# Optimization experiments

Hardware: AMD Instinct MI355X
Metric: run time of the kernel (lower is better)

Reference implementation:

```python
import jax, jax.numpy as jnp
import numpy as np

B, T, IN, OUT, H, N, M = 16, 1024, 64, 64, 512, 128, 40
EPS = 1e-8


def setup_inputs() -> dict:
    key = jax.random.key(0)
    ks = jax.random.split(key, 16)
    s = 0.02  # xavier-ish init scale for weights
    inp = {
        "x": jax.random.normal(ks[0], (B, T, IN), jnp.float32),
        "h0": jnp.zeros((B, H), jnp.float32),
        "c0": jnp.zeros((B, H), jnp.float32),
        "memory0": jax.random.normal(ks[1], (B, N, M), jnp.float32) * 0.01,
        "read0": jnp.zeros((B, M), jnp.float32),
        # LSTMCell params (torch gate order: i, f, g, o)
        "W_ih": jax.random.normal(ks[2], (4 * H, IN + M), jnp.float32) * s,
        "b_ih": jnp.zeros((4 * H,), jnp.float32),
        "W_hh": jax.random.normal(ks[3], (4 * H, H), jnp.float32) * s,
        "b_hh": jnp.zeros((4 * H,), jnp.float32),
        "W_fc": jax.random.normal(ks[4], (OUT, H), jnp.float32) * s,
        "b_fc": jnp.zeros((OUT,), jnp.float32),
        "W_e": jax.random.normal(ks[5], (M, H), jnp.float32) * s,
        "b_e": jnp.zeros((M,), jnp.float32),
        "W_a": jax.random.normal(ks[6], (M, H), jnp.float32) * s,
        "b_a": jnp.zeros((M,), jnp.float32),
        "W_k": jax.random.normal(ks[7], (M, H), jnp.float32) * s,
        "b_k": jnp.zeros((M,), jnp.float32),
        "W_b": jax.random.normal(ks[8], (1, H), jnp.float32) * s,
        "b_b": jnp.zeros((1,), jnp.float32),
    }
    return inp


def _ntm_scan(x, h0, c0, memory0, read0, W_ih, b_ih, W_hh, b_hh,
              W_fc, b_fc, W_e, b_e, W_a, b_a, W_k, b_k, W_b, b_b):
    def step(carry, x_t):
        h, c, mem, r = carry
        # controller LSTM cell on [x_t, read_vector]
        inp = jnp.concatenate([x_t, r], axis=-1)            # [B, IN+M]
        gates = inp @ W_ih.T + b_ih + h @ W_hh.T + b_hh      # [B, 4H]
        i, f, g, o = jnp.split(gates, 4, axis=-1)
        i = jax.nn.sigmoid(i); f = jax.nn.sigmoid(f)
        g = jnp.tanh(g);       o = jax.nn.sigmoid(o)
        c = f * c + i * g
        h = o * jnp.tanh(c)
        out = jnp.tanh(h @ W_fc.T + b_fc)                    # [B, OUT]
        # content addressing
        key = jnp.tanh(h @ W_k.T + b_k)                      # [B, M]
        beta = jax.nn.softplus(h @ W_b.T + b_b) + EPS        # [B, 1]
        kn = key / (jnp.linalg.norm(key, axis=-1, keepdims=True) + EPS)
        mn = mem / (jnp.linalg.norm(mem, axis=-1, keepdims=True) + EPS)
        sim = jnp.einsum('bnm,bm->bn', mn, kn)               # [B, N]
        w = jax.nn.softmax(beta * sim, axis=-1)              # [B, N]
        # erase/add write, then read from updated memory
        e = jax.nn.sigmoid(h @ W_e.T + b_e)                  # [B, M]
        a = jnp.tanh(h @ W_a.T + b_a)                        # [B, M]
        mem = mem * (1.0 - w[:, :, None] * e[:, None, :]) + w[:, :, None] * a[:, None, :]
        r = jnp.einsum('bn,bnm->bm', w, mem)                 # [B, M]
        return (h, c, mem, r), out

    xs = jnp.swapaxes(x, 0, 1)                               # [T, B, IN]
    (h, c, mem, r), outs = jax.lax.scan(step, (h0, c0, memory0, read0), xs)
    return jnp.swapaxes(outs, 0, 1), h, c                    # [B, T, OUT]


def reference(x, h0, c0, memory0, read0, W_ih, b_ih, W_hh, b_hh,
              W_fc, b_fc, W_e, b_e, W_a, b_a, W_k, b_k, W_b, b_b):
    return _ntm_scan(x, h0, c0, memory0, read0, W_ih, b_ih, W_hh, b_hh,
                     W_fc, b_fc, W_e, b_e, W_a, b_a, W_k, b_k, W_b, b_b)
```

## Files before the change

kernel.cpp:

```cpp
#include <hip/hip_runtime.h>
#include <math.h>

#define Bq   16
#define Tq   1024
#define OUTq 64
#define Hq   512
#define Nq   128
#define Mq   40
#define NT   512
#define NISL 16
#define GWG  13
#define IWG  14
#define NWG  224
#define EPSq 1e-8f
#define MAGIC 0x00C0FFEEu

typedef unsigned long long ull;

__device__ __forceinline__ float sigmf(float x){ return 1.f/(1.f + expf(-x)); }
__device__ __forceinline__ float softplusf(float x){ return (x > 20.f) ? x : log1pf(expf(x)); }

__device__ __forceinline__ ull icld64(const ull* p){
  return __hip_atomic_load(p, __ATOMIC_RELAXED, __HIP_MEMORY_SCOPE_AGENT);
}
__device__ __forceinline__ void icst64(ull* p, ull v){
  __hip_atomic_store(p, v, __ATOMIC_RELAXED, __HIP_MEMORY_SCOPE_AGENT);
}
__device__ __forceinline__ ull icpoll64(const ull* p){
  ull v;
  asm volatile("global_load_dwordx2 %0, %1, off sc0 sc1\n\ts_waitcnt vmcnt(0)"
               : "=v"(v) : "v"(p) : "memory");
  return v;
}
__device__ __forceinline__ ull packtv(unsigned tag, float v){
  return ((ull)tag << 32) | (ull)__float_as_uint(v);
}
__device__ __forceinline__ float lowf(ull v){ return __uint_as_float((unsigned)v); }

__device__ __forceinline__ float waitword(const ull* sh, unsigned want, bool fast){
  if (fast){
    #pragma unroll 1
    for (int i = 0; i < 4096; ++i){
      const ull v = icpoll64(sh);
      if ((unsigned)(v >> 32) == want) return lowf(v);
      __builtin_amdgcn_s_sleep(1);
    }
  }
  #pragma unroll 1
  for (;;){
    const ull v = icld64(sh);
    if ((unsigned)(v >> 32) == want) return lowf(v);
    __builtin_amdgcn_s_sleep(1);
  }
}

__device__ __forceinline__ int ready_and_handshake(ull* rdy, ull* magic, int blk){
  __hip_atomic_fetch_add(rdy, 1ull, __ATOMIC_RELAXED, __HIP_MEMORY_SCOPE_AGENT);
  while (icld64(rdy) < (ull)NWG) __builtin_amdgcn_s_sleep(8);
  if (blk == 0) icst64(magic, ((ull)MAGIC << 32) | 1ull);
  #pragma unroll 1
  for (int i = 0; i < 4000; ++i){
    if ((unsigned)(icpoll64(magic) >> 32) == MAGIC) return 1;
    __builtin_amdgcn_s_sleep(2);
  }
  return 0;
}

extern "C" __global__ void __launch_bounds__(NT, 1)
ntm_kernel(const float* __restrict__ xg,  const float* __restrict__ h0g,
           const float* __restrict__ c0g, const float* __restrict__ mem0g,
           const float* __restrict__ read0g,
           const float* __restrict__ Wih, const float* __restrict__ bih,
           const float* __restrict__ Whh, const float* __restrict__ bhh,
           const float* __restrict__ Wfc, const float* __restrict__ bfc,
           const float* __restrict__ We,  const float* __restrict__ be,
           const float* __restrict__ Wa,  const float* __restrict__ ba,
           const float* __restrict__ Wk,  const float* __restrict__ bk,
           const float* __restrict__ Wb,  const float* __restrict__ bbeta,
           float* __restrict__ yout, ull* __restrict__ rdy,
           ull* __restrict__ h_sh, ull* __restrict__ r_sh)
{
  const int blk = blockIdx.x;
  const int tid = threadIdx.x;
  const int x   = blk & 7;
  const int j   = blk >> 3;
  const int bat = (j < IWG) ? x : (x + 8);
  const int slot= (j < IWG) ? j : (j - IWG);
  __shared__ __align__(16) char smem[41344];
  __shared__ int s_fast;
  ull* magic = rdy + 1;

  if (slot < GWG){
    float* inp_s  = (float*)smem;
    float* red_s  = (float*)(smem + 2560);
    float* rw_s   = (float*)(smem + 13440);
    float* r_s    = (float*)(smem + 39680);
    float* gate_s = (float*)(smem + 39840);
    float* c_s    = (float*)(smem + 40480);
    float* bias_s = (float*)(smem + 40640);

    const int kseg  = tid & 15;
    const int rslot = tid >> 4;
    const int nd    = (slot < 12) ? 40 : 32;
    const int d0    = slot * 40;
    const int rowsR = 4 * nd;

    float4 w4[5][9];
    #pragma unroll
    for (int rr = 0; rr < 5; ++rr){
      const int row = rslot*5 + rr;
      if (row < rowsR){
        const int gate = row / nd, ld = row - gate*nd;
        const int grow = gate*Hq + d0 + ld;
        #pragma unroll
        for (int kk = 0; kk < 9; ++kk){
          float v[4];
          #pragma unroll
          for (int c4 = 0; c4 < 4; ++c4){
            const int k = kseg*36 + kk*4 + c4;
            v[c4] = (k < 64) ? Wih[grow*104 + k] : Whh[grow*512 + (k - 64)];
          }
          w4[rr][kk] = make_float4(v[0], v[1], v[2], v[3]);
        }
      } else {
        #pragma unroll
        for (int kk = 0; kk < 9; ++kk) w4[rr][kk] = make_float4(0.f,0.f,0.f,0.f);
      }
    }
    if (tid < rowsR){
      const int gate = tid / nd, ld = tid - gate*nd;
      const int grow = gate*Hq + d0 + ld;
      bias_s[tid] = bih[grow] + bhh[grow];
    }
    for (int i = tid; i < rowsR*40; i += NT){
      const int row = i / 40, m = i - row*40;
      const int gate = row / nd, ld = row - gate*nd;
      const int grow = gate*Hq + d0 + ld;
      rw_s[row*41 + m] = Wih[grow*104 + 64 + m];
    }
    if (tid < nd) c_s[tid] = c0g[bat*Hq + d0 + tid];
    if (tid < 16)
      *(float4*)&inp_s[tid*4] = ((const float4*)xg)[(bat*Tq + 0)*16 + tid];
    if (tid < 128)
      *(float4*)&inp_s[64 + tid*4] = ((const float4*)h0g)[bat*128 + tid];
    __syncthreads();
    if (tid == 0) s_fast = ready_and_handshake(rdy, magic, blk);
    __syncthreads();
    const bool fast = (s_fast != 0);

    for (int t = 0; t < Tq; ++t){
      const int p = t & 1, pm = (t - 1) & 1;
      float acc[5] = {0.f,0.f,0.f,0.f,0.f};
      {
        const float* bp = inp_s + kseg*36;
        #pragma unroll
        for (int kk = 0; kk < 9; ++kk){
          const float4 f = *(const float4*)&bp[kk*4];
          #pragma unroll
          for (int rr = 0; rr < 5; ++rr)
            acc[rr] += w4[rr][kk].x*f.x + w4[rr][kk].y*f.y
                     + w4[rr][kk].z*f.z + w4[rr][kk].w*f.w;
        }
      }
      #pragma unroll
      for (int rr = 0; rr < 5; ++rr)
        red_s[(rslot*5 + rr)*17 + kseg] = acc[rr];
      if (t == 0){
        if (tid < 40) r_s[tid] = read0g[bat*Mq + tid];
      } else if (tid < 40){
        const int idx = (pm*NISL + bat)*Mq + tid;
        r_s[tid] = waitword(&r_sh[idx], (unsigned)t, fast);
      }
      __syncthreads();
      if (tid < rowsR){
        float s2 = bias_s[tid];
        const float* rp = &red_s[tid*17];
        #pragma unroll
        for (int q = 0; q < 16; ++q) s2 += rp[q];
        const float* rwp = &rw_s[tid*41];
        #pragma unroll
        for (int m = 0; m < 40; ++m) s2 += rwp[m]*r_s[m];
        gate_s[tid] = s2;
      }
      __syncthreads();
      if (tid < nd){
        const float gi = gate_s[tid];
        const float gf = gate_s[nd + tid];
        const float gc = gate_s[2*nd + tid];
        const float go = gate_s[3*nd + tid];
        const float iv = sigmf(gi), fv = sigmf(gf), gv = tanhf(gc), ov = sigmf(go);
        const float cn = fv*c_s[tid] + iv*gv;
        const float hn = ov*tanhf(cn);
        c_s[tid] = cn;
        const int idx = (p*NISL + bat)*Hq + d0 + tid;
        icst64(&h_sh[idx], packtv((unsigned)(t+1), hn));
        if (t == Tq - 1){
          yout[Bq*Tq*OUTq + bat*Hq + d0 + tid] = hn;
          yout[Bq*Tq*OUTq + Bq*Hq + bat*Hq + d0 + tid] = cn;
        }
      }
      {
        const int idx = (p*NISL + bat)*Hq + tid;
        inp_s[64 + tid] = waitword(&h_sh[idx], (unsigned)(t+1), fast);
      }
      if (t + 1 < Tq && tid < 16)
        *(float4*)&inp_s[tid*4] = ((const float4*)xg)[(bat*Tq + t + 1)*16 + tid];
      __syncthreads();
    }
  }
  else {
    float* mem_s  = (float*)smem;
    float* h_s    = (float*)(smem + 22528);
    float* hred_s = (float*)(smem + 24576);
    float* key_s  = (float*)(smem + 26624);
    float* e_s    = (float*)(smem + 26784);
    float* a_s    = (float*)(smem + 26944);
    float* w_s    = (float*)(smem + 27104);
    float* rred_s = (float*)(smem + 27616);
    float* ored_s = (float*)(smem + 29056);

    #pragma unroll
    for (int q = 0; q < 10; ++q){
      const int e = q*512 + tid;
      const int n = e / 40, m = e - n*40;
      mem_s[n*44 + m] = mem0g[bat*(Nq*Mq) + e];
    }
    const int o  = tid & 127;
    const int kc = tid >> 7;
    const float* wrow = (o < 40) ? (Wk + o*Hq)
                      : (o < 80) ? (We + (o-40)*Hq)
                      : (o < 120) ? (Wa + (o-80)*Hq)
                      : (o == 120) ? Wb : nullptr;
    float4 wv2[32];
    if (wrow){
      #pragma unroll
      for (int kk = 0; kk < 32; ++kk)
        wv2[kk] = *(const float4*)&wrow[kc*128 + kk*4];
    } else {
      #pragma unroll
      for (int kk = 0; kk < 32; ++kk) wv2[kk] = make_float4(0.f,0.f,0.f,0.f);
    }
    float4 wfc[16];
    {
      const int o2 = tid & 63, kc8 = tid >> 6;
      #pragma unroll
      for (int kk = 0; kk < 16; ++kk)
        wfc[kk] = *(const float4*)&Wfc[o2*Hq + kc8*64 + kk*4];
    }
    const float bfcv = bfc[tid & 63];
    float hb0 = 0.f, hb1 = 0.f;
    if (tid < 64){
      const int o0 = tid, o1 = tid + 64;
      hb0 = (o0 < 40) ? bk[o0] : be[o0-40];
      hb1 = (o1 < 80) ? be[o1-40] : (o1 < 120) ? ba[o1-80]
          : (o1 == 120) ? bbeta[0] : 0.f;
    }
    __syncthreads();
    if (tid == 0) s_fast = ready_and_handshake(rdy, magic, blk);
    __syncthreads();
    const bool fast = (s_fast != 0);

    for (int t = 0; t < Tq; ++t){
      const int p = t & 1;
      const unsigned want = (unsigned)(t + 1);
      {
        const int idx = (p*NISL + bat)*Hq + tid;
        h_s[tid] = waitword(&h_sh[idx], want, fast);
      }
      __syncthreads();
      {
        float a0 = 0.f;
        const float* hp = h_s + kc*128;
        #pragma unroll
        for (int kk = 0; kk < 32; ++kk){
          const float4 f = *(const float4*)&hp[kk*4];
          a0 += wv2[kk].x*f.x + wv2[kk].y*f.y + wv2[kk].z*f.z + wv2[kk].w*f.w;
        }
        hred_s[o*4 + kc] = a0;
      }
      __syncthreads();
      if (tid < 64){
        const int l = tid;
        const float4 p0 = *(const float4*)&hred_s[l*4];
        const float4 p1 = *(const float4*)&hred_s[(l+64)*4];
        float s0 = hb0 + p0.x + p0.y + p0.z + p0.w;
        float s1 = hb1 + p1.x + p1.y + p1.z + p1.w;
        float kv = 0.f;
        if (l < 40){ kv = tanhf(s0); key_s[l] = kv; }
        else        { e_s[l-40] = sigmf(s0); }
        if (l < 16)      e_s[l+24]  = sigmf(s1);
        else if (l < 56) a_s[l-16]  = tanhf(s1);
        float bval = softplusf(s1) + EPSq;
        const float bet = __shfl(bval, 56);
        float ss = kv*kv;
        #pragma unroll
        for (int off = 32; off; off >>= 1) ss += __shfl_xor(ss, off);
        const float rinv = 1.f/(sqrtf(ss) + EPSq);
        float sc[2];
        #pragma unroll
        for (int half = 0; half < 2; ++half){
          const int n = l + 64*half;
          float qq = 0.f, dd = 0.f;
          const float* mrow = &mem_s[n*44];
          #pragma unroll
          for (int q = 0; q < 10; ++q){
            const float4 mv = *(const float4*)&mrow[q*4];
            const float4 kvv = *(const float4*)&key_s[q*4];
            qq += mv.x*mv.x + mv.y*mv.y + mv.z*mv.z + mv.w*mv.w;
            dd += mv.x*kvv.x + mv.y*kvv.y + mv.z*kvv.z + mv.w*kvv.w;
          }
          sc[half] = bet * dd * rinv / (sqrtf(qq) + EPSq);
        }
        const float e0 = expf(sc[0]), e1 = expf(sc[1]);
        float sm = e0 + e1;
        #pragma unroll
        for (int off = 32; off; off >>= 1) sm += __shfl_xor(sm, off);
        const float inv = 1.f/sm;
        w_s[l] = e0*inv; w_s[l+64] = e1*inv;
      }
      __syncthreads();
      if (tid < 320){
        const int m = tid % 40, ng = tid / 40;
        const float ev = e_s[m], av = a_s[m];
        float part = 0.f;
        #pragma unroll
        for (int q = 0; q < 16; ++q){
          const int n = ng*16 + q, idx2 = n*44 + m;
          const float mv = mem_s[idx2];
          const float wn = w_s[n];
          const float nv = fmaf(wn, fmaf(-ev, mv, av), mv);
          mem_s[idx2] = nv;
          part = fmaf(wn, nv, part);
        }
        rred_s[m*9 + ng] = part;
      }
      __syncthreads();
      if (tid < 40){
        float r = 0.f;
        #pragma unroll
        for (int q = 0; q < 8; ++q) r += rred_s[tid*9 + q];
        const int idx = (p*NISL + bat)*Mq + tid;
        icst64(&r_sh[idx], packtv(want, r));
      }
      {
        const int o2 = tid & 63, kc8 = tid >> 6;
        float a0 = 0.f;
        const float* hp = h_s + kc8*64;
        #pragma unroll
        for (int kk = 0; kk < 16; ++kk){
          const float4 f = *(const float4*)&hp[kk*4];
          a0 += wfc[kk].x*f.x + wfc[kk].y*f.y + wfc[kk].z*f.z + wfc[kk].w*f.w;
        }
        ored_s[o2*9 + kc8] = a0;
      }
      __syncthreads();
      if (tid < 64){
        float s2 = bfcv;
        const float* op = &ored_s[tid*9];
        #pragma unroll
        for (int q = 0; q < 8; ++q) s2 += op[q];
        yout[(bat*Tq + t)*OUTq + tid] = tanhf(s2);
      }
      __syncthreads();
    }
  }
}

extern "C" void kernel_launch(void* const* d_in, const int* in_sizes, int n_in,
                              void* d_out, int out_size, void* d_ws, size_t ws_size,
                              hipStream_t stream){
  const float* xg    = (const float*)d_in[0];
  const float* h0g   = (const float*)d_in[1];
  const float* c0g   = (const float*)d_in[2];
  const float* mem0g = (const float*)d_in[3];
  const float* read0g= (const float*)d_in[4];
  const float* Wih   = (const float*)d_in[5];
  const float* bih   = (const float*)d_in[6];
  const float* Whh   = (const float*)d_in[7];
  const float* bhh   = (const float*)d_in[8];
  const float* Wfc   = (const float*)d_in[9];
  const float* bfc   = (const float*)d_in[10];
  const float* We    = (const float*)d_in[11];
  const float* be    = (const float*)d_in[12];
  const float* Wa    = (const float*)d_in[13];
  const float* ba    = (const float*)d_in[14];
  const float* Wk    = (const float*)d_in[15];
  const float* bk    = (const float*)d_in[16];
  const float* Wb    = (const float*)d_in[17];
  const float* bbeta = (const float*)d_in[18];

  float* yout  = (float*)d_out;
  ull*   rdy   = (ull*)d_ws;
  ull*   h_sh  = (ull*)((char*)d_ws + 4096);
  ull*   r_sh  = (ull*)((char*)d_ws + 135168);

  hipMemsetAsync(d_ws, 0, 147456, stream);
  hipLaunchKernelGGL(ntm_kernel, dim3(NWG), dim3(NT), 0, stream,
                     xg, h0g, c0g, mem0g, read0g, Wih, bih, Whh, bhh,
                     Wfc, bfc, We, be, Wa, ba, Wk, bk, Wb, bbeta,
                     yout, rdy, h_sh, r_sh);
}
```

Before: 6.419 ms.

## Compute head projections as partial sums in LSTM workgroups, reduce in memory workgroup

Each gate workgroup now computes partial dot products of its own slice of h with the key/erase/add/beta weight rows and publishes them to a new global flag-tagged buffer. The memory workgroup sums the 13 partials instead of waiting for the full h and doing the 512-wide projection, which shortens the critical recurrent path. The full-h wait moves later, used only for the output FC, and one trailing barrier is dropped. This adds an extra block barrier and more global atomic stores in the gate workgroups, plus 13 polls per projection row.

```diff
diff --git a/kernel.cpp b/kernel.cpp
--- a/kernel.cpp
+++ b/kernel.cpp
@@ -78,7 +78,8 @@
            const float* __restrict__ Wk,  const float* __restrict__ bk,
            const float* __restrict__ Wb,  const float* __restrict__ bbeta,
            float* __restrict__ yout, ull* __restrict__ rdy,
-           ull* __restrict__ h_sh, ull* __restrict__ r_sh)
+           ull* __restrict__ h_sh, ull* __restrict__ r_sh,
+           ull* __restrict__ hp_sh)
 {
   const int blk = blockIdx.x;
   const int tid = threadIdx.x;
@@ -104,6 +105,9 @@
     const int nd    = (slot < 12) ? 40 : 32;
     const int d0    = slot * 40;
     const int rowsR = 4 * nd;
+    const int prow  = tid >> 2;
+    const int pq    = tid & 3;
+    const int ncol  = nd >> 2;
 
     float4 w4[5][9];
     #pragma unroll
@@ -126,6 +130,17 @@
         #pragma unroll
         for (int kk = 0; kk < 9; ++kk) w4[rr][kk] = make_float4(0.f,0.f,0.f,0.f);
       }
+    }
+    float hw[10];
+    #pragma unroll
+    for (int c = 0; c < 10; ++c) hw[c] = 0.f;
+    if (prow < 121){
+      const float* wsrc = (prow < 40) ? (Wk + prow*Hq)
+                        : (prow < 80) ? (We + (prow-40)*Hq)
+                        : (prow < 120) ? (Wa + (prow-80)*Hq) : Wb;
+      #pragma unroll
+      for (int c = 0; c < 10; ++c)
+        if (c < ncol) hw[c] = wsrc[d0 + pq*ncol + c];
     }
     if (tid < rowsR){
       const int gate = tid / nd, ld = tid - gate*nd;
@@ -192,11 +207,25 @@
         const float cn = fv*c_s[tid] + iv*gv;
         const float hn = ov*tanhf(cn);
         c_s[tid] = cn;
+        r_s[tid] = hn;
         const int idx = (p*NISL + bat)*Hq + d0 + tid;
         icst64(&h_sh[idx], packtv((unsigned)(t+1), hn));
         if (t == Tq - 1){
           yout[Bq*Tq*OUTq + bat*Hq + d0 + tid] = hn;
           yout[Bq*Tq*OUTq + Bq*Hq + bat*Hq + d0 + tid] = cn;
+        }
+      }
+      __syncthreads();
+      {
+        float ps = 0.f;
+        #pragma unroll
+        for (int c = 0; c < 10; ++c)
+          if (c < ncol) ps = fmaf(hw[c], r_s[pq*ncol + c], ps);
+        ps += __shfl_xor(ps, 1);
+        ps += __shfl_xor(ps, 2);
+        if (prow < 121 && pq == 0){
+          const int hidx = ((p*NISL + bat)*GWG + slot)*128 + prow;
+          icst64(&hp_sh[hidx], packtv((unsigned)(t+1), ps));
         }
       }
       {
@@ -225,21 +254,8 @@
       const int n = e / 40, m = e - n*40;
       mem_s[n*44 + m] = mem0g[bat*(Nq*Mq) + e];
     }
-    const int o  = tid & 127;
-    const int kc = tid >> 7;
-    const float* wrow = (o < 40) ? (Wk + o*Hq)
-                      : (o < 80) ? (We + (o-40)*Hq)
-                      : (o < 120) ? (Wa + (o-80)*Hq)
-                      : (o == 120) ? Wb : nullptr;
-    float4 wv2[32];
-    if (wrow){
-      #pragma unroll
-      for (int kk = 0; kk < 32; ++kk)
-        wv2[kk] = *(const float4*)&wrow[kc*128 + kk*4];
-    } else {
-      #pragma unroll
-      for (int kk = 0; kk < 32; ++kk) wv2[kk] = make_float4(0.f,0.f,0.f,0.f);
-    }
+    const int prow_m = tid & 127;
+    const int psg    = tid >> 7;
     float4 wfc[16];
     {
       const int o2 = tid & 63, kc8 = tid >> 6;
@@ -263,20 +279,18 @@
     for (int t = 0; t < Tq; ++t){
       const int p = t & 1;
       const unsigned want = (unsigned)(t + 1);
-      {
-        const int idx = (p*NISL + bat)*Hq + tid;
-        h_s[tid] = waitword(&h_sh[idx], want, fast);
-      }
-      __syncthreads();
-      {
-        float a0 = 0.f;
-        const float* hp = h_s + kc*128;
-        #pragma unroll
-        for (int kk = 0; kk < 32; ++kk){
-          const float4 f = *(const float4*)&hp[kk*4];
-          a0 += wv2[kk].x*f.x + wv2[kk].y*f.y + wv2[kk].z*f.z + wv2[kk].w*f.w;
-        }
-        hred_s[o*4 + kc] = a0;
+      if (prow_m < 121){
+        const int sbase = (psg == 0) ? 0 : (psg*3 + 1);
+        const int scnt  = (psg == 0) ? 4 : 3;
+        float s = 0.f;
+        #pragma unroll
+        for (int ss = 0; ss < 4; ++ss){
+          if (ss < scnt){
+            const int hidx = ((p*NISL + bat)*GWG + (sbase + ss))*128 + prow_m;
+            s += waitword(&hp_sh[hidx], want, fast);
+          }
+        }
+        hred_s[prow_m*4 + psg] = s;
       }
       __syncthreads();
       if (tid < 64){
@@ -343,6 +357,11 @@
         icst64(&r_sh[idx], packtv(want, r));
       }
       {
+        const int idx = (p*NISL + bat)*Hq + tid;
+        h_s[tid] = waitword(&h_sh[idx], want, fast);
+      }
+      __syncthreads();
+      {
         const int o2 = tid & 63, kc8 = tid >> 6;
         float a0 = 0.f;
         const float* hp = h_s + kc8*64;
@@ -361,7 +380,6 @@
         for (int q = 0; q < 8; ++q) s2 += op[q];
         yout[(bat*Tq + t)*OUTq + tid] = tanhf(s2);
       }
-      __syncthreads();
     }
   }
 }
@@ -393,10 +411,11 @@
   ull*   rdy   = (ull*)d_ws;
   ull*   h_sh  = (ull*)((char*)d_ws + 4096);
   ull*   r_sh  = (ull*)((char*)d_ws + 135168);
-
-  hipMemsetAsync(d_ws, 0, 147456, stream);
+  ull*   hp_sh = (ull*)((char*)d_ws + 147456);
+
+  hipMemsetAsync(d_ws, 0, 573440, stream);
   hipLaunchKernelGGL(ntm_kernel, dim3(NWG), dim3(NT), 0, stream,
                      xg, h0g, c0g, mem0g, read0g, Wih, bih, Whh, bhh,
                      Wfc, bfc, We, be, Wa, ba, Wk, bk, Wb, bbeta,
-                     yout, rdy, h_sh, r_sh);
-}
+                     yout, rdy, h_sh, r_sh, hp_sh);
+}
```

New measurement: 6.982 ms. 8.8% more time.

## Replace per-word tagged handoff with packed data plus per-batch arrival counters

Applied to the files above, without the earlier changes.

Cross-workgroup exchange of h and the read vector used to put a step tag next to every float, so each consumer polled every word. Now two floats share each 64-bit word and producers bump a per-batch atomic counter after a vmcnt wait. Consumers poll one counter, then read the packed data once. This cuts the traffic and polling on the serial critical path. It depends on ordering between the data stores and the counter increment, and it also drops a trailing __syncthreads in the memory workgroup.

```diff
diff --git a/kernel.cpp b/kernel.cpp
--- a/kernel.cpp
+++ b/kernel.cpp
@@ -32,26 +32,31 @@
                : "=v"(v) : "v"(p) : "memory");
   return v;
 }
-__device__ __forceinline__ ull packtv(unsigned tag, float v){
-  return ((ull)tag << 32) | (ull)__float_as_uint(v);
+__device__ __forceinline__ ull rd64(const ull* p, bool fast){
+  return fast ? icpoll64(p) : icld64(p);
+}
+__device__ __forceinline__ ull pack2(float lo, float hi){
+  return ((ull)__float_as_uint(hi) << 32) | (ull)__float_as_uint(lo);
 }
 __device__ __forceinline__ float lowf(ull v){ return __uint_as_float((unsigned)v); }
-
-__device__ __forceinline__ float waitword(const ull* sh, unsigned want, bool fast){
+__device__ __forceinline__ float highf(ull v){ return __uint_as_float((unsigned)(v >> 32)); }
+
+__device__ __forceinline__ void pollcnt(const ull* c, ull target, bool fast){
   if (fast){
     #pragma unroll 1
-    for (int i = 0; i < 4096; ++i){
-      const ull v = icpoll64(sh);
-      if ((unsigned)(v >> 32) == want) return lowf(v);
+    for (int i = 0; i < (1 << 22); ++i){
+      if (icpoll64(c) >= target) return;
       __builtin_amdgcn_s_sleep(1);
     }
   }
   #pragma unroll 1
   for (;;){
-    const ull v = icld64(sh);
-    if ((unsigned)(v >> 32) == want) return lowf(v);
+    if (icld64(c) >= target) return;
     __builtin_amdgcn_s_sleep(1);
   }
+}
+__device__ __forceinline__ void cntbump(ull* c){
+  __hip_atomic_fetch_add(c, 1ull, __ATOMIC_RELAXED, __HIP_MEMORY_SCOPE_AGENT);
 }
 
 __device__ __forceinline__ int ready_and_handshake(ull* rdy, ull* magic, int blk){
@@ -78,7 +83,8 @@
            const float* __restrict__ Wk,  const float* __restrict__ bk,
            const float* __restrict__ Wb,  const float* __restrict__ bbeta,
            float* __restrict__ yout, ull* __restrict__ rdy,
-           ull* __restrict__ h_sh, ull* __restrict__ r_sh)
+           ull* __restrict__ h_dat, ull* __restrict__ r_dat,
+           ull* __restrict__ h_cnt, ull* __restrict__ r_cnt)
 {
   const int blk = blockIdx.x;
   const int tid = threadIdx.x;
@@ -89,6 +95,8 @@
   __shared__ __align__(16) char smem[41344];
   __shared__ int s_fast;
   ull* magic = rdy + 1;
+  ull* hc = h_cnt + bat*16;
+  ull* rc = r_cnt + bat*16;
 
   if (slot < GWG){
     float* inp_s  = (float*)smem;
@@ -167,9 +175,12 @@
         red_s[(rslot*5 + rr)*17 + kseg] = acc[rr];
       if (t == 0){
         if (tid < 40) r_s[tid] = read0g[bat*Mq + tid];
-      } else if (tid < 40){
-        const int idx = (pm*NISL + bat)*Mq + tid;
-        r_s[tid] = waitword(&r_sh[idx], (unsigned)t, fast);
+      } else {
+        pollcnt(rc, (ull)t, fast);
+        if (tid < 20){
+          const ull w = rd64(&r_dat[(pm*NISL + bat)*32 + tid], fast);
+          r_s[2*tid] = lowf(w); r_s[2*tid + 1] = highf(w);
+        }
       }
       __syncthreads();
       if (tid < rowsR){
@@ -183,25 +194,33 @@
         gate_s[tid] = s2;
       }
       __syncthreads();
-      if (tid < nd){
-        const float gi = gate_s[tid];
-        const float gf = gate_s[nd + tid];
-        const float gc = gate_s[2*nd + tid];
-        const float go = gate_s[3*nd + tid];
-        const float iv = sigmf(gi), fv = sigmf(gf), gv = tanhf(gc), ov = sigmf(go);
-        const float cn = fv*c_s[tid] + iv*gv;
-        const float hn = ov*tanhf(cn);
-        c_s[tid] = cn;
-        const int idx = (p*NISL + bat)*Hq + d0 + tid;
-        icst64(&h_sh[idx], packtv((unsigned)(t+1), hn));
-        if (t == Tq - 1){
-          yout[Bq*Tq*OUTq + bat*Hq + d0 + tid] = hn;
-          yout[Bq*Tq*OUTq + Bq*Hq + bat*Hq + d0 + tid] = cn;
-        }
-      }
-      {
-        const int idx = (p*NISL + bat)*Hq + tid;
-        inp_s[64 + tid] = waitword(&h_sh[idx], (unsigned)(t+1), fast);
+      if (tid < 64){
+        float hn = 0.f;
+        if (tid < nd){
+          const float gi = gate_s[tid];
+          const float gf = gate_s[nd + tid];
+          const float gc = gate_s[2*nd + tid];
+          const float go = gate_s[3*nd + tid];
+          const float iv = sigmf(gi), fv = sigmf(gf), gv = tanhf(gc), ov = sigmf(go);
+          const float cn = fv*c_s[tid] + iv*gv;
+          hn = ov*tanhf(cn);
+          c_s[tid] = cn;
+          if (t == Tq - 1){
+            yout[Bq*Tq*OUTq + bat*Hq + d0 + tid] = hn;
+            yout[Bq*Tq*OUTq + Bq*Hq + bat*Hq + d0 + tid] = cn;
+          }
+        }
+        const float lo = __shfl(hn, 2*tid);
+        const float hi = __shfl(hn, 2*tid + 1);
+        if (tid < (nd >> 1))
+          icst64(&h_dat[(p*NISL + bat)*256 + (d0 >> 1) + tid], pack2(lo, hi));
+        asm volatile("s_waitcnt vmcnt(0)" ::: "memory");
+        if (tid == 0) cntbump(hc);
+      }
+      pollcnt(hc, (ull)(13*(t + 1)), fast);
+      if (tid < 256){
+        const ull w = rd64(&h_dat[(p*NISL + bat)*256 + tid], fast);
+        inp_s[64 + 2*tid] = lowf(w); inp_s[64 + 2*tid + 1] = highf(w);
       }
       if (t + 1 < Tq && tid < 16)
         *(float4*)&inp_s[tid*4] = ((const float4*)xg)[(bat*Tq + t + 1)*16 + tid];
@@ -262,10 +281,10 @@
 
     for (int t = 0; t < Tq; ++t){
       const int p = t & 1;
-      const unsigned want = (unsigned)(t + 1);
-      {
-        const int idx = (p*NISL + bat)*Hq + tid;
-        h_s[tid] = waitword(&h_sh[idx], want, fast);
+      pollcnt(hc, (ull)(13*(t + 1)), fast);
+      if (tid < 256){
+        const ull w = rd64(&h_dat[(p*NISL + bat)*256 + tid], fast);
+        h_s[2*tid] = lowf(w); h_s[2*tid + 1] = highf(w);
       }
       __syncthreads();
       {
@@ -335,12 +354,18 @@
         rred_s[m*9 + ng] = part;
       }
       __syncthreads();
-      if (tid < 40){
+      if (tid < 64){
         float r = 0.f;
-        #pragma unroll
-        for (int q = 0; q < 8; ++q) r += rred_s[tid*9 + q];
-        const int idx = (p*NISL + bat)*Mq + tid;
-        icst64(&r_sh[idx], packtv(want, r));
+        if (tid < 40){
+          #pragma unroll
+          for (int q = 0; q < 8; ++q) r += rred_s[tid*9 + q];
+        }
+        const float lo = __shfl(r, 2*tid);
+        const float hi = __shfl(r, 2*tid + 1);
+        if (tid < 20)
+          icst64(&r_dat[(p*NISL + bat)*32 + tid], pack2(lo, hi));
+        asm volatile("s_waitcnt vmcnt(0)" ::: "memory");
+        if (tid == 0) cntbump(rc);
       }
       {
         const int o2 = tid & 63, kc8 = tid >> 6;
@@ -361,7 +386,6 @@
         for (int q = 0; q < 8; ++q) s2 += op[q];
         yout[(bat*Tq + t)*OUTq + tid] = tanhf(s2);
       }
-      __syncthreads();
     }
   }
 }
@@ -391,12 +415,14 @@
 
   float* yout  = (float*)d_out;
   ull*   rdy   = (ull*)d_ws;
-  ull*   h_sh  = (ull*)((char*)d_ws + 4096);
-  ull*   r_sh  = (ull*)((char*)d_ws + 135168);
-
-  hipMemsetAsync(d_ws, 0, 147456, stream);
+  ull*   h_dat = (ull*)((char*)d_ws + 4096);
+  ull*   r_dat = (ull*)((char*)d_ws + 69632);
+  ull*   h_cnt = (ull*)((char*)d_ws + 77824);
+  ull*   r_cnt = (ull*)((char*)d_ws + 79872);
+
+  hipMemsetAsync(d_ws, 0, 81920, stream);
   hipLaunchKernelGGL(ntm_kernel, dim3(NWG), dim3(NT), 0, stream,
                      xg, h0g, c0g, mem0g, read0g, Wih, bih, Whh, bhh,
                      Wfc, bfc, We, be, Wa, ba, Wk, bk, Wb, bbeta,
-                     yout, rdy, h_sh, r_sh);
-}
+                     yout, rdy, h_dat, r_dat, h_cnt, r_cnt);
+}
```

Measured after the change: 10.23 ms. 1.59x slower.

## Process two batch rows per workgroup, halving the persistent grid

Applied to the files above, without the earlier changes.

Each workgroup now handles two batch elements (pr and pr+8) instead of one, so the grid shrinks from 224 to 112 workgroups. The register-resident weight slices are reused for both batches, shared memory grows to hold duplicated per-batch buffers, and the polling and reduction phases are split across thread halves. This reduces the number of workgroups taking part in the cross-workgroup spin synchronisation each step and doubles weight reuse. The cost is more serial work per workgroup on the critical path of every timestep.

```diff
diff --git a/kernel.cpp b/kernel.cpp
--- a/kernel.cpp
+++ b/kernel.cpp
@@ -11,7 +11,7 @@
 #define NISL 16
 #define GWG  13
 #define IWG  14
-#define NWG  224
+#define NWG  112
 #define EPSq 1e-8f
 #define MAGIC 0x00C0FFEEu
 
@@ -82,22 +82,27 @@
 {
   const int blk = blockIdx.x;
   const int tid = threadIdx.x;
-  const int x   = blk & 7;
+  const int pr  = blk & 7;
   const int j   = blk >> 3;
-  const int bat = (j < IWG) ? x : (x + 8);
-  const int slot= (j < IWG) ? j : (j - IWG);
-  __shared__ __align__(16) char smem[41344];
+  const int batA = pr, batB = pr + 8;
+  const int slot = j;
+  __shared__ __align__(16) char smem[62720];
   __shared__ int s_fast;
   ull* magic = rdy + 1;
 
   if (slot < GWG){
-    float* inp_s  = (float*)smem;
-    float* red_s  = (float*)(smem + 2560);
-    float* rw_s   = (float*)(smem + 13440);
-    float* r_s    = (float*)(smem + 39680);
-    float* gate_s = (float*)(smem + 39840);
-    float* c_s    = (float*)(smem + 40480);
-    float* bias_s = (float*)(smem + 40640);
+    float* inp_sA = (float*)smem;
+    float* inp_sB = (float*)(smem + 2560);
+    float* red_sA = (float*)(smem + 5120);
+    float* red_sB = (float*)(smem + 16000);
+    float* rw_s   = (float*)(smem + 26880);
+    float* r_sA   = (float*)(smem + 53120);
+    float* r_sB   = (float*)(smem + 53280);
+    float* gate_sA= (float*)(smem + 53440);
+    float* gate_sB= (float*)(smem + 54080);
+    float* c_sA   = (float*)(smem + 54720);
+    float* c_sB   = (float*)(smem + 54880);
+    float* bias_s = (float*)(smem + 55040);
 
     const int kseg  = tid & 15;
     const int rslot = tid >> 4;
@@ -138,11 +143,18 @@
       const int grow = gate*Hq + d0 + ld;
       rw_s[row*41 + m] = Wih[grow*104 + 64 + m];
     }
-    if (tid < nd) c_s[tid] = c0g[bat*Hq + d0 + tid];
+    if (tid < nd){
+      c_sA[tid] = c0g[batA*Hq + d0 + tid];
+      c_sB[tid] = c0g[batB*Hq + d0 + tid];
+    }
     if (tid < 16)
-      *(float4*)&inp_s[tid*4] = ((const float4*)xg)[(bat*Tq + 0)*16 + tid];
+      *(float4*)&inp_sA[tid*4] = ((const float4*)xg)[(batA*Tq + 0)*16 + tid];
+    else if (tid < 32)
+      *(float4*)&inp_sB[(tid-16)*4] = ((const float4*)xg)[(batB*Tq + 0)*16 + tid-16];
     if (tid < 128)
-      *(float4*)&inp_s[64 + tid*4] = ((const float4*)h0g)[bat*128 + tid];
+      *(float4*)&inp_sA[64 + tid*4] = ((const float4*)h0g)[batA*128 + tid];
+    else if (tid < 256)
+      *(float4*)&inp_sB[64 + (tid-128)*4] = ((const float4*)h0g)[batB*128 + (tid-128)];
     __syncthreads();
     if (tid == 0) s_fast = ready_and_handshake(rdy, magic, blk);
     __syncthreads();
@@ -150,9 +162,9 @@
 
     for (int t = 0; t < Tq; ++t){
       const int p = t & 1, pm = (t - 1) & 1;
-      float acc[5] = {0.f,0.f,0.f,0.f,0.f};
       {
-        const float* bp = inp_s + kseg*36;
+        float acc[5] = {0.f,0.f,0.f,0.f,0.f};
+        const float* bp = inp_sA + kseg*36;
         #pragma unroll
         for (int kk = 0; kk < 9; ++kk){
           const float4 f = *(const float4*)&bp[kk*4];
@@ -161,69 +173,130 @@
             acc[rr] += w4[rr][kk].x*f.x + w4[rr][kk].y*f.y
                      + w4[rr][kk].z*f.z + w4[rr][kk].w*f.w;
         }
-      }
-      #pragma unroll
-      for (int rr = 0; rr < 5; ++rr)
-        red_s[(rslot*5 + rr)*17 + kseg] = acc[rr];
+        #pragma unroll
+        for (int rr = 0; rr < 5; ++rr)
+          red_sA[(rslot*5 + rr)*17 + kseg] = acc[rr];
+      }
+      {
+        float acc[5] = {0.f,0.f,0.f,0.f,0.f};
+        const float* bp = inp_sB + kseg*36;
+        #pragma unroll
+        for (int kk = 0; kk < 9; ++kk){
+          const float4 f = *(const float4*)&bp[kk*4];
+          #pragma unroll
+          for (int rr = 0; rr < 5; ++rr)
+            acc[rr] += w4[rr][kk].x*f.x + w4[rr][kk].y*f.y
+                     + w4[rr][kk].z*f.z + w4[rr][kk].w*f.w;
+        }
+        #pragma unroll
+        for (int rr = 0; rr < 5; ++rr)
+          red_sB[(rslot*5 + rr)*17 + kseg] = acc[rr];
+      }
       if (t == 0){
-        if (tid < 40) r_s[tid] = read0g[bat*Mq + tid];
-      } else if (tid < 40){
-        const int idx = (pm*NISL + bat)*Mq + tid;
-        r_s[tid] = waitword(&r_sh[idx], (unsigned)t, fast);
+        if (tid < 40) r_sA[tid] = read0g[batA*Mq + tid];
+        else if (tid >= 64 && tid < 104) r_sB[tid-64] = read0g[batB*Mq + (tid-64)];
+      } else {
+        if (tid < 40)
+          r_sA[tid] = waitword(&r_sh[(pm*NISL + batA)*Mq + tid], (unsigned)t, fast);
+        else if (tid >= 64 && tid < 104)
+          r_sB[tid-64] = waitword(&r_sh[(pm*NISL + batB)*Mq + (tid-64)], (unsigned)t, fast);
       }
       __syncthreads();
       if (tid < rowsR){
         float s2 = bias_s[tid];
-        const float* rp = &red_s[tid*17];
+        const float* rp = &red_sA[tid*17];
         #pragma unroll
         for (int q = 0; q < 16; ++q) s2 += rp[q];
         const float* rwp = &rw_s[tid*41];
         #pragma unroll
-        for (int m = 0; m < 40; ++m) s2 += rwp[m]*r_s[m];
-        gate_s[tid] = s2;
+        for (int m = 0; m < 40; ++m) s2 += rwp[m]*r_sA[m];
+        gate_sA[tid] = s2;
+      } else if (tid >= 256 && tid < 256 + rowsR){
+        const int row = tid - 256;
+        float s2 = bias_s[row];
+        const float* rp = &red_sB[row*17];
+        #pragma unroll
+        for (int q = 0; q < 16; ++q) s2 += rp[q];
+        const float* rwp = &rw_s[row*41];
+        #pragma unroll
+        for (int m = 0; m < 40; ++m) s2 += rwp[m]*r_sB[m];
+        gate_sB[row] = s2;
       }
       __syncthreads();
       if (tid < nd){
-        const float gi = gate_s[tid];
-        const float gf = gate_s[nd + tid];
-        const float gc = gate_s[2*nd + tid];
-        const float go = gate_s[3*nd + tid];
+        const float gi = gate_sA[tid];
+        const float gf = gate_sA[nd + tid];
+        const float gc = gate_sA[2*nd + tid];
+        const float go = gate_sA[3*nd + tid];
         const float iv = sigmf(gi), fv = sigmf(gf), gv = tanhf(gc), ov = sigmf(go);
-        const float cn = fv*c_s[tid] + iv*gv;
+        const float cn = fv*c_sA[tid] + iv*gv;
         const float hn = ov*tanhf(cn);
-        c_s[tid] = cn;
-        const int idx = (p*NISL + bat)*Hq + d0 + tid;
-        icst64(&h_sh[idx], packtv((unsigned)(t+1), hn));
+        c_sA[tid] = cn;
+        icst64(&h_sh[(p*NISL + batA)*Hq + d0 + tid], packtv((unsigned)(t+1), hn));
         if (t == Tq - 1){
-          yout[Bq*Tq*OUTq + bat*Hq + d0 + tid] = hn;
-          yout[Bq*Tq*OUTq + Bq*Hq + bat*Hq + d0 + tid] = cn;
-        }
-      }
-      {
-        const int idx = (p*NISL + bat)*Hq + tid;
-        inp_s[64 + tid] = waitword(&h_sh[idx], (unsigned)(t+1), fast);
-      }
-      if (t + 1 < Tq && tid < 16)
-        *(float4*)&inp_s[tid*4] = ((const float4*)xg)[(bat*Tq + t + 1)*16 + tid];
+          yout[Bq*Tq*OUTq + batA*Hq + d0 + tid] = hn;
+          yout[Bq*Tq*OUTq + Bq*Hq + batA*Hq + d0 + tid] = cn;
+        }
+      } else if (tid >= 64 && tid < 64 + nd){
+        const int ld = tid - 64;
+        const float gi = gate_sB[ld];
+        const float gf = gate_sB[nd + ld];
+        const float gc = gate_sB[2*nd + ld];
+        const float go = gate_sB[3*nd + ld];
+        const float iv = sigmf(gi), fv = sigmf(gf), gv = tanhf(gc), ov = sigmf(go);
+        const float cn = fv*c_sB[ld] + iv*gv;
+        const float hn = ov*tanhf(cn);
+        c_sB[ld] = cn;
+        icst64(&h_sh[(p*NISL + batB)*Hq + d0 + ld], packtv((unsigned)(t+1), hn));
+        if (t == Tq - 1){
+          yout[Bq*Tq*OUTq + batB*Hq + d0 + ld] = hn;
+          yout[Bq*Tq*OUTq + Bq*Hq + batB*Hq + d0 + ld] = cn;
+        }
+      }
+      if (tid < 256){
+        const int i0 = 2*tid;
+        inp_sA[64 + i0]     = waitword(&h_sh[(p*NISL + batA)*Hq + i0],     (unsigned)(t+1), fast);
+        inp_sA[64 + i0 + 1] = waitword(&h_sh[(p*NISL + batA)*Hq + i0 + 1], (unsigned)(t+1), fast);
+      } else {
+        const int i0 = 2*(tid - 256);
+        inp_sB[64 + i0]     = waitword(&h_sh[(p*NISL + batB)*Hq + i0],     (unsigned)(t+1), fast);
+        inp_sB[64 + i0 + 1] = waitword(&h_sh[(p*NISL + batB)*Hq + i0 + 1], (unsigned)(t+1), fast);
+      }
+      if (t + 1 < Tq){
+        if (tid < 16)
+          *(float4*)&inp_sA[tid*4] = ((const float4*)xg)[(batA*Tq + t + 1)*16 + tid];
+        else if (tid < 32)
+          *(float4*)&inp_sB[(tid-16)*4] = ((const float4*)xg)[(batB*Tq + t + 1)*16 + (tid-16)];
+      }
       __syncthreads();
     }
   }
   else {
-    float* mem_s  = (float*)smem;
-    float* h_s    = (float*)(smem + 22528);
-    float* hred_s = (float*)(smem + 24576);
-    float* key_s  = (float*)(smem + 26624);
-    float* e_s    = (float*)(smem + 26784);
-    float* a_s    = (float*)(smem + 26944);
-    float* w_s    = (float*)(smem + 27104);
-    float* rred_s = (float*)(smem + 27616);
-    float* ored_s = (float*)(smem + 29056);
+    float* mem_sA = (float*)smem;
+    float* mem_sB = (float*)(smem + 22528);
+    float* h_sA   = (float*)(smem + 45056);
+    float* h_sB   = (float*)(smem + 47104);
+    float* hredA  = (float*)(smem + 49152);
+    float* hredB  = (float*)(smem + 51200);
+    float* keyA   = (float*)(smem + 53248);
+    float* keyB   = (float*)(smem + 53408);
+    float* eA     = (float*)(smem + 53568);
+    float* eB     = (float*)(smem + 53728);
+    float* aA     = (float*)(smem + 53888);
+    float* aB     = (float*)(smem + 54048);
+    float* w_sA   = (float*)(smem + 54208);
+    float* w_sB   = (float*)(smem + 54720);
+    float* rredA  = (float*)(smem + 55232);
+    float* rredB  = (float*)(smem + 56672);
+    float* oredA  = (float*)(smem + 58112);
+    float* oredB  = (float*)(smem + 60416);
 
     #pragma unroll
     for (int q = 0; q < 10; ++q){
       const int e = q*512 + tid;
       const int n = e / 40, m = e - n*40;
-      mem_s[n*44 + m] = mem0g[bat*(Nq*Mq) + e];
+      mem_sA[n*44 + m] = mem0g[batA*(Nq*Mq) + e];
+      mem_sB[n*44 + m] = mem0g[batB*(Nq*Mq) + e];
     }
     const int o  = tid & 127;
     const int kc = tid >> 7;
@@ -249,9 +322,10 @@
     }
     const float bfcv = bfc[tid & 63];
     float hb0 = 0.f, hb1 = 0.f;
-    if (tid < 64){
-      const int o0 = tid, o1 = tid + 64;
-      hb0 = (o0 < 40) ? bk[o0] : be[o0-40];
+    if (tid < 128){
+      const int l = tid & 63;
+      const int o1 = l + 64;
+      hb0 = (l < 40) ? bk[l] : be[l-40];
       hb1 = (o1 < 80) ? be[o1-40] : (o1 < 120) ? ba[o1-80]
           : (o1 == 120) ? bbeta[0] : 0.f;
     }
@@ -263,26 +337,45 @@
     for (int t = 0; t < Tq; ++t){
       const int p = t & 1;
       const unsigned want = (unsigned)(t + 1);
-      {
-        const int idx = (p*NISL + bat)*Hq + tid;
-        h_s[tid] = waitword(&h_sh[idx], want, fast);
+      if (tid < 256){
+        const int i0 = 2*tid;
+        h_sA[i0]     = waitword(&h_sh[(p*NISL + batA)*Hq + i0],     want, fast);
+        h_sA[i0 + 1] = waitword(&h_sh[(p*NISL + batA)*Hq + i0 + 1], want, fast);
+      } else {
+        const int i0 = 2*(tid - 256);
+        h_sB[i0]     = waitword(&h_sh[(p*NISL + batB)*Hq + i0],     want, fast);
+        h_sB[i0 + 1] = waitword(&h_sh[(p*NISL + batB)*Hq + i0 + 1], want, fast);
       }
       __syncthreads();
       {
         float a0 = 0.f;
-        const float* hp = h_s + kc*128;
+        const float* hp = h_sA + kc*128;
         #pragma unroll
         for (int kk = 0; kk < 32; ++kk){
           const float4 f = *(const float4*)&hp[kk*4];
           a0 += wv2[kk].x*f.x + wv2[kk].y*f.y + wv2[kk].z*f.z + wv2[kk].w*f.w;
         }
-        hred_s[o*4 + kc] = a0;
-      }
-      __syncthreads();
-      if (tid < 64){
-        const int l = tid;
-        const float4 p0 = *(const float4*)&hred_s[l*4];
-        const float4 p1 = *(const float4*)&hred_s[(l+64)*4];
+        hredA[o*4 + kc] = a0;
+        float b0 = 0.f;
+        const float* hq = h_sB + kc*128;
+        #pragma unroll
+        for (int kk = 0; kk < 32; ++kk){
+          const float4 f = *(const float4*)&hq[kk*4];
+          b0 += wv2[kk].x*f.x + wv2[kk].y*f.y + wv2[kk].z*f.z + wv2[kk].w*f.w;
+        }
+        hredB[o*4 + kc] = b0;
+      }
+      __syncthreads();
+      if (tid < 128){
+        const int l = tid & 63;
+        float* hred = (tid < 64) ? hredA : hredB;
+        float* key_s= (tid < 64) ? keyA  : keyB;
+        float* e_s  = (tid < 64) ? eA    : eB;
+        float* a_s  = (tid < 64) ? aA    : aB;
+        float* w_s  = (tid < 64) ? w_sA  : w_sB;
+        float* mem_s= (tid < 64) ? mem_sA: mem_sB;
+        const float4 p0 = *(const float4*)&hred[l*4];
+        const float4 p1 = *(const float4*)&hred[(l+64)*4];
         float s0 = hb0 + p0.x + p0.y + p0.z + p0.w;
         float s1 = hb1 + p1.x + p1.y + p1.z + p1.w;
         float kv = 0.f;
@@ -321,45 +414,76 @@
       __syncthreads();
       if (tid < 320){
         const int m = tid % 40, ng = tid / 40;
-        const float ev = e_s[m], av = a_s[m];
-        float part = 0.f;
-        #pragma unroll
-        for (int q = 0; q < 16; ++q){
-          const int n = ng*16 + q, idx2 = n*44 + m;
-          const float mv = mem_s[idx2];
-          const float wn = w_s[n];
-          const float nv = fmaf(wn, fmaf(-ev, mv, av), mv);
-          mem_s[idx2] = nv;
-          part = fmaf(wn, nv, part);
-        }
-        rred_s[m*9 + ng] = part;
+        {
+          const float ev = eA[m], av = aA[m];
+          float part = 0.f;
+          #pragma unroll
+          for (int q = 0; q < 16; ++q){
+            const int n = ng*16 + q, idx2 = n*44 + m;
+            const float mv = mem_sA[idx2];
+            const float wn = w_sA[n];
+            const float nv = fmaf(wn, fmaf(-ev, mv, av), mv);
+            mem_sA[idx2] = nv;
+            part = fmaf(wn, nv, part);
+          }
+          rredA[m*9 + ng] = part;
+        }
+        {
+          const float ev = eB[m], av = aB[m];
+          float part = 0.f;
+          #pragma unroll
+          for (int q = 0; q < 16; ++q){
+            const int n = ng*16 + q, idx2 = n*44 + m;
+            const float mv = mem_sB[idx2];
+            const float wn = w_sB[n];
+            const float nv = fmaf(wn, fmaf(-ev, mv, av), mv);
+            mem_sB[idx2] = nv;
+            part = fmaf(wn, nv, part);
+          }
+          rredB[m*9 + ng] = part;
+        }
       }
       __syncthreads();
       if (tid < 40){
         float r = 0.f;
         #pragma unroll
-        for (int q = 0; q < 8; ++q) r += rred_s[tid*9 + q];
-        const int idx = (p*NISL + bat)*Mq + tid;
-        icst64(&r_sh[idx], packtv(want, r));
+        for (int q = 0; q < 8; ++q) r += rredA[tid*9 + q];
+        icst64(&r_sh[(p*NISL + batA)*Mq + tid], packtv(want, r));
+      } else if (tid >= 64 && tid < 104){
+        const int ld = tid - 64;
+        float r = 0.f;
+        #pragma unroll
+        for (int q = 0; q < 8; ++q) r += rredB[ld*9 + q];
+        icst64(&r_sh[(p*NISL + batB)*Mq + ld], packtv(want, r));
       }
       {
         const int o2 = tid & 63, kc8 = tid >> 6;
         float a0 = 0.f;
-        const float* hp = h_s + kc8*64;
+        const float* hp = h_sA + kc8*64;
         #pragma unroll
         for (int kk = 0; kk < 16; ++kk){
           const float4 f = *(const float4*)&hp[kk*4];
           a0 += wfc[kk].x*f.x + wfc[kk].y*f.y + wfc[kk].z*f.z + wfc[kk].w*f.w;
         }
-        ored_s[o2*9 + kc8] = a0;
-      }
-      __syncthreads();
-      if (tid < 64){
+        oredA[o2*9 + kc8] = a0;
+        float b0 = 0.f;
+        const float* hq = h_sB + kc8*64;
+        #pragma unroll
+        for (int kk = 0; kk < 16; ++kk){
+          const float4 f = *(const float4*)&hq[kk*4];
+          b0 += wfc[kk].x*f.x + wfc[kk].y*f.y + wfc[kk].z*f.z + wfc[kk].w*f.w;
+        }
+        oredB[o2*9 + kc8] = b0;
+      }
+      __syncthreads();
+      if (tid < 128){
+        const int l = tid & 63;
+        const float* op = (tid < 64) ? &oredA[l*9] : &oredB[l*9];
+        const int bat = (tid < 64) ? batA : batB;
         float s2 = bfcv;
-        const float* op = &ored_s[tid*9];
         #pragma unroll
         for (int q = 0; q < 8; ++q) s2 += op[q];
-        yout[(bat*Tq + t)*OUTq + tid] = tanhf(s2);
+        yout[(bat*Tq + t)*OUTq + l] = tanhf(s2);
       }
       __syncthreads();
     }
```

Result: slower. 10.59 ms (+65.0%).
